# Optimization experiments

Hardware: AMD Instinct MI355X
Metric: run time of the kernel (lower is better)

The kernel has to match this reference:

```python
import jax, jax.numpy as jnp
import numpy as np

ROPE_BASE = 10000.0


def _rope(x):
    # x: (B, S, H, D) -- rotate-half RoPE applied per head over the sequence dim
    B, S, H, D = x.shape
    half = D // 2
    inv_freq = 1.0 / (ROPE_BASE ** (jnp.arange(half, dtype=jnp.float32) / half))
    ang = jnp.arange(S, dtype=jnp.float32)[:, None] * inv_freq[None, :]  # (S, half)
    cos = jnp.cos(ang)[None, :, None, :].astype(x.dtype)
    sin = jnp.sin(ang)[None, :, None, :].astype(x.dtype)
    x1, x2 = x[..., :half], x[..., half:]
    return jnp.concatenate([x1 * cos - x2 * sin, x2 * cos + x1 * sin], axis=-1)


def setup_inputs() -> dict:
    key = jax.random.key(0)
    ks = jax.random.split(key, 7)
    B, S, D = 8, 1024, 512
    HD = 512  # num_heads * key_dim = 8 * 64
    scale = 0.02
    return {
        "query": jax.random.normal(ks[0], (B, S, D), dtype=jnp.float32),
        "value": jax.random.normal(ks[1], (B, S, D), dtype=jnp.float32),
        "key_in": jax.random.normal(ks[2], (B, S, D), dtype=jnp.float32),
        "Wq": jax.random.normal(ks[3], (D, HD), dtype=jnp.float32) * scale,
        "Wk": jax.random.normal(ks[4], (D, HD), dtype=jnp.float32) * scale,
        "Wv": jax.random.normal(ks[5], (D, HD), dtype=jnp.float32) * scale,
        "Wo": jax.random.normal(ks[6], (HD, D), dtype=jnp.float32) * scale,
    }


def reference(query, value, key_in, Wq, Wk, Wv, Wo):
    H, Dh = 8, 64
    B, Sq, _ = query.shape
    Sk = key_in.shape[1]
    # QKV projections, split heads: (B, S, H, Dh)
    q = (query @ Wq).reshape(B, Sq, H, Dh)
    v = (value @ Wv).reshape(B, Sk, H, Dh)
    k = (key_in @ Wk).reshape(B, Sk, H, Dh)
    # inline RoPE on q and k (applied before head transpose, as in the original)
    q = _rope(q)
    k = _rope(k)
    # scaled dot-product attention with causal mask
    q = q * (1.0 / jnp.sqrt(jnp.asarray(Dh, q.dtype)))
    scores = jnp.einsum("bqhd,bkhd->bhqk", q, k)  # (B, H, Sq, Sk)
    causal = jnp.tril(jnp.ones((Sq, Sk), dtype=bool))[None, None]
    scores = jnp.where(causal, scores, jnp.asarray(-1e9, scores.dtype))
    probs = jax.nn.softmax(scores, axis=-1)
    out = jnp.einsum("bhqk,bkhd->bqhd", probs, v)  # (B, Sq, H, Dh)
    out = out.reshape(B, Sq, H * Dh) @ Wo  # output projection
    return out
```

## Files before the change

kernel.cpp:

```cpp
#include <hip/hip_runtime.h>
#include <hip/hip_bf16.h>
#include <stdint.h>

#define DEV static __device__ __forceinline__

typedef __attribute__((ext_vector_type(8)))  short    s16x8;
typedef __attribute__((ext_vector_type(4)))  short    s16x4;
typedef __attribute__((ext_vector_type(8)))  __bf16   bf16x8;
typedef __attribute__((ext_vector_type(4)))  float    f32x4;
typedef __attribute__((ext_vector_type(16))) float    f32x16;
typedef __attribute__((ext_vector_type(2)))  unsigned u32x2;
typedef __attribute__((ext_vector_type(4)))  unsigned u32x4;

DEV short f2b(float f){
  union{float f; uint32_t i;} x; x.f = f;
  uint32_t r = x.i + 0x7FFFu + ((x.i >> 16) & 1u);
  return (short)(r >> 16);
}
DEV bf16x8 as_bf(s16x8 v){ return __builtin_bit_cast(bf16x8, v); }
DEV float fexp2(float x){ return __builtin_amdgcn_exp2f(x); }
DEV f32x4 mf(s16x8 a, s16x8 b, f32x4 c){
  return __builtin_amdgcn_mfma_f32_16x16x32_bf16(as_bf(a), as_bf(b), c, 0, 0, 0);
}
DEV f32x16 mf32(s16x8 a, s16x8 b, f32x16 c){
  return __builtin_amdgcn_mfma_f32_32x32x16_bf16(as_bf(a), as_bf(b), c, 0, 0, 0);
}

DEV void gload_lds16(const void* g, void* l){
  __builtin_amdgcn_global_load_lds((const __attribute__((address_space(1))) void*)g,
                                   (__attribute__((address_space(3))) void*)l, 16, 0, 0);
}

#if __has_builtin(__builtin_amdgcn_permlane32_swap)
DEV void pswap2(unsigned a, unsigned b, unsigned& x, unsigned& y){
  u32x2 rr = __builtin_amdgcn_permlane32_swap(a, b, false, false);
  x = rr[0]; y = rr[1];
}
DEV float partner32(float v, int hi){
  unsigned u = __builtin_bit_cast(unsigned, v);
  u32x2 rr = __builtin_amdgcn_permlane32_swap(u, u, false, false);
  return __builtin_bit_cast(float, hi ? rr[0] : rr[1]);
}
#else
DEV void pswap2(unsigned a, unsigned b, unsigned& x, unsigned& y){
  unsigned pa_ = (unsigned)__shfl_xor((int)a, 32, 64);
  unsigned pb_ = (unsigned)__shfl_xor((int)b, 32, 64);
  int lo = ((threadIdx.x & 63) < 32);
  x = lo ? a   : pb_;
  y = lo ? pa_ : b;
}
DEV float partner32(float v, int hi){ (void)hi; return __shfl_xor(v, 32, 64); }
#endif

__global__ __launch_bounds__(256) void k_conv3(const float* __restrict__ q,
                                               const float* __restrict__ k,
                                               const float* __restrict__ v,
                                               short* __restrict__ out){
  int z = blockIdx.z;
  const float* in = (z == 0) ? q : (z == 1) ? k : v;
  int i = (blockIdx.x * 256 + threadIdx.x) * 4;
  float4 val = *(const float4*)(in + i);
  short o[4] = { f2b(val.x), f2b(val.y), f2b(val.z), f2b(val.w) };
  *(uint2*)(out + (size_t)z * 4194304 + i) = *(uint2*)o;
}

__global__ __launch_bounds__(256) void k_wt4(const float* __restrict__ w0,
                                             const float* __restrict__ w1,
                                             const float* __restrict__ w2,
                                             const float* __restrict__ w3,
                                             short* __restrict__ wt){
  __shared__ float tile[32][33];
  int z = blockIdx.z;
  const float* w = (z == 0) ? w0 : (z == 1) ? w1 : (z == 2) ? w2 : w3;
  short* o = wt + (size_t)z * 262144;
  int bx = blockIdx.x * 32, by = blockIdx.y * 32;
  int tx = threadIdx.x, ty = threadIdx.y;
  for (int j = 0; j < 32; j += 8)
    tile[ty + j][tx] = w[(size_t)(by + ty + j) * 512 + bx + tx];
  __syncthreads();
  for (int j = 0; j < 32; j += 8)
    o[(size_t)(bx + ty + j) * 512 + by + tx] = f2b(tile[tx][ty + j]);
}

__global__ __launch_bounds__(256) void k_table(float* __restrict__ tab){
  int idx = blockIdx.x * 256 + threadIdx.x;
  int s = idx >> 5, j = idx & 31;
  float inv = __expf(-(float)j * (1.0f / 32.0f) * logf(10000.0f));
  float ang = (float)s * inv;
  tab[idx * 2 + 0] = cosf(ang);
  tab[idx * 2 + 1] = sinf(ang);
}

__global__ __launch_bounds__(256) void k_qkv(const short* __restrict__ Xb,
                                             const short* __restrict__ Wcat,
                                             const float* __restrict__ tab,
                                             short* __restrict__ Qa,
                                             short* __restrict__ Ka,
                                             short* __restrict__ Vt){
  __shared__ __align__(16) short Al[2][4096];
  __shared__ __align__(16) short Bl[2][4096];
  const int t = threadIdx.x, w = t >> 6, lane = t & 63, fr = lane & 15, fg = lane >> 4;
  const int sel = blockIdx.y >> 2;
  const short* X = Xb + (size_t)sel * 4194304;
  const int bm = blockIdx.x * 128, bn = blockIdx.y * 128;
  const int wm = (w >> 1) * 64, wn = (w & 1) * 64;

  auto stage = [&](int buf, int k0){
#pragma unroll
    for (int q = 0; q < 2; q++){
      int lin = q * 256 + t;
      int row = lin >> 2, sl = lin & 3;
      int gs = (sl ^ (row & 3)) * 8;
      gload_lds16(X    + (size_t)(bm + row) * 512 + k0 + gs, &Al[buf][(q * 256 + w * 64) * 8]);
      gload_lds16(Wcat + (size_t)(bn + row) * 512 + k0 + gs, &Bl[buf][(q * 256 + w * 64) * 8]);
    }
  };

  f32x4 acc[4][4] = {};
  stage(0, 0);
  __syncthreads();
  int cur = 0;
  for (int t16 = 0; t16 < 16; ++t16){
    if (t16 < 15) stage(cur ^ 1, (t16 + 1) * 32);
    s16x8 af[4], bv[4];
#pragma unroll
    for (int f = 0; f < 4; f++){
      int ra = wm + f * 16 + fr;
      af[f] = *(const s16x8*)(&Al[cur][ra * 32 + ((fg ^ (ra & 3)) * 8)]);
      int rb = wn + f * 16 + fr;
      bv[f] = *(const s16x8*)(&Bl[cur][rb * 32 + ((fg ^ (rb & 3)) * 8)]);
    }
#pragma unroll
    for (int i = 0; i < 4; i++)
#pragma unroll
      for (int jj = 0; jj < 4; jj++)
        acc[i][jj] = mf(af[i], bv[jj], acc[i][jj]);
    __syncthreads();
    cur ^= 1;
  }

  const int row0 = bm + wm + fg * 4;
  const int b = row0 >> 10;
  const int s_base = row0 & 1023;
  const int hh = (((blockIdx.y & 3) * 128) + wn) >> 6;
  if (sel < 2){
    const float scale = (sel == 0) ? 0.125f * 1.44269504f : 1.0f;
    short* out = (sel == 0) ? Qa : Ka;
#pragma unroll
    for (int i = 0; i < 4; i++)
#pragma unroll
      for (int jj = 0; jj < 2; jj++){
        int d = jj * 16 + fr;
#pragma unroll
        for (int r = 0; r < 4; r++){
          int s = s_base + i * 16 + r;
          float2 cs = *(const float2*)(tab + (size_t)(s * 32 + d) * 2);
          float x1 = acc[i][jj][r], x2 = acc[i][jj + 2][r];
          size_t ob = ((size_t)((b * 8 + hh) * 1024 + s)) * 64 + d;
          out[ob]      = f2b((x1 * cs.x - x2 * cs.y) * scale);
          out[ob + 32] = f2b((x2 * cs.x + x1 * cs.y) * scale);
        }
      }
  } else {
#pragma unroll
    for (int i = 0; i < 4; i++)
#pragma unroll
      for (int jj = 0; jj < 4; jj++){
        int d = jj * 16 + fr;
        s16x4 pk;
#pragma unroll
        for (int r = 0; r < 4; r++) pk[r] = f2b(acc[i][jj][r]);
        size_t ob = ((size_t)((b * 8 + hh) * 64 + d)) * 1024 + s_base + i * 16;
        *(s16x4*)(Vt + ob) = pk;
      }
  }
}

__global__ __launch_bounds__(128) void k_attn(const short* __restrict__ Qb,
                                              const short* __restrict__ Kb,
                                              const short* __restrict__ Vt,
                                              short* __restrict__ O){
  __shared__ __align__(16) short KL[2][4096];
  __shared__ __align__(16) short VL[2][4096];
  const int bid = blockIdx.x;
  const int podr[16] = {15,14,13,12, 0,1,2,3, 11,10,9,8, 4,5,6,7};
  const int Bi = podr[bid >> 6];
  const int bh = bid & 63;
  const int B0 = Bi * 64;
  const int t = threadIdx.x, w = t >> 6, lane = t & 63;
  const int col = lane & 31, hi = lane >> 5;
  const short* Qp = Qb + (size_t)bh * 65536;
  const short* Kp = Kb + (size_t)bh * 65536;
  const short* Vp = Vt + (size_t)bh * 65536;
  const int qrow = B0 + 2 * col + w;

  s16x8 qb[4];
#pragma unroll
  for (int ks = 0; ks < 4; ks++)
    qb[ks] = *(const s16x8*)(Qp + (size_t)qrow * 64 + ks * 16 + hi * 8);

  int crow[16];
#pragma unroll
  for (int r = 0; r < 16; r++) crow[r] = (r & 3) + 8 * (r >> 2) + 4 * hi;

  f32x16 oacc[2] = {};
  float m = -1e30f, l = 0.f;

  auto stage = [&](int buf, int kv0){
#pragma unroll
    for (int R = 0; R < 4; R++){
      int lin = R * 128 + w * 64 + lane;
      int row = lin >> 3, slot = lin & 7;
      int gs = ((slot ^ (row & 7)) * 8);
      gload_lds16(Kp + (size_t)(kv0 + row) * 64 + gs, &KL[buf][(R * 128 + w * 64) * 8]);
      gload_lds16(Vp + (size_t)row * 1024 + kv0 + gs, &VL[buf][(R * 128 + w * 64) * 8]);
    }
  };

  stage(0, 0);
  __syncthreads();

  int cur = 0;
  for (int kv0 = 0; kv0 <= B0; kv0 += 64){
    if (kv0 < B0) stage(cur ^ 1, kv0 + 64);
    f32x16 sc[2];
#pragma unroll
    for (int f = 0; f < 2; f++){
      f32x16 s = {};
      int row = f * 32 + col, rx = row & 7;
#pragma unroll
      for (int ks = 0; ks < 4; ks++){
        s16x8 ka = *(const s16x8*)(&KL[cur][row * 64 + ((ks * 2 + hi) ^ rx) * 8]);
        s = mf32(ka, qb[ks], s);
      }
      sc[f] = s;
    }
    if (kv0 == B0){
#pragma unroll
      for (int f = 0; f < 2; f++)
#pragma unroll
        for (int r = 0; r < 16; r++){
          int kv = kv0 + f * 32 + crow[r];
          if (kv > qrow) sc[f][r] = -1e30f;
        }
    }
    float tm = -1e30f;
#pragma unroll
    for (int f = 0; f < 2; f++)
#pragma unroll
      for (int r = 0; r < 16; r++) tm = fmaxf(tm, sc[f][r]);
    tm = fmaxf(tm, partner32(tm, hi));
    if (!__all(tm <= m + 8.f)){
      float mn = fmaxf(m, tm);
      float corr = fexp2(m - mn);
      m = mn;
      l *= corr;
      float cpv[16];
#pragma unroll
      for (int r = 0; r < 16; r++) cpv[r] = __shfl(corr, crow[r], 64);
#pragma unroll
      for (int r = 0; r < 16; r++){ oacc[0][r] *= cpv[r]; oacc[1][r] *= cpv[r]; }
    }
    float rs = 0.f;
    unsigned wq[2][8];
#pragma unroll
    for (int f = 0; f < 2; f++)
#pragma unroll
      for (int i = 0; i < 8; i++){
        float p0 = fexp2(sc[f][2 * i]     - m);
        float p1 = fexp2(sc[f][2 * i + 1] - m);
        rs += p0 + p1;
        wq[f][i] = (unsigned)(uint16_t)f2b(p0) | ((unsigned)(uint16_t)f2b(p1) << 16);
      }
    rs += partner32(rs, hi);
    l += rs;
    s16x8 pa[4];
#pragma unroll
    for (int f = 0; f < 2; f++)
#pragma unroll
      for (int half = 0; half < 2; half++){
        unsigned w0, w1, w2, w3;
        pswap2(wq[f][half * 4 + 0], wq[f][half * 4 + 2], w0, w2);
        pswap2(wq[f][half * 4 + 1], wq[f][half * 4 + 3], w1, w3);
        u32x4 uv = { w0, w1, w2, w3 };
        pa[f * 2 + half] = __builtin_bit_cast(s16x8, uv);
      }
#pragma unroll
    for (int ks = 0; ks < 4; ks++)
#pragma unroll
      for (int df = 0; df < 2; df++){
        int row = df * 32 + col;
        s16x8 vb = *(const s16x8*)(&VL[cur][row * 64 + ((ks * 2 + hi) ^ (row & 7)) * 8]);
        oacc[df] = mf32(pa[ks], vb, oacc[df]);
      }
    if (kv0 < B0) __syncthreads();
    cur ^= 1;
  }

  const int b = bh >> 3, h = bh & 7;
  float lf[16];
#pragma unroll
  for (int r = 0; r < 16; r++) lf[r] = __shfl(l, crow[r], 64);
#pragma unroll
  for (int r = 0; r < 16; r++){
    int qq = B0 + 2 * crow[r] + w;
    float inv = 1.0f / lf[r];
    O[(size_t)(b * 1024 + qq) * 512 + h * 64 + col]      = f2b(oacc[0][r] * inv);
    O[(size_t)(b * 1024 + qq) * 512 + h * 64 + 32 + col] = f2b(oacc[1][r] * inv);
  }
}

__global__ __launch_bounds__(256, 2) void k_gemm_out(const short* __restrict__ X,
                                                     const short* __restrict__ Wt,
                                                     float* __restrict__ C){
  __shared__ __align__(16) short Al[2][8192];
  __shared__ __align__(16) short Bl[2][8192];
  const int t = threadIdx.x;
  const int w = t >> 6, lane = t & 63, fr = lane & 15, fg = lane >> 4;
  const int bm = blockIdx.x * 128, bn = blockIdx.y * 128;
  const int wm = (w >> 1) * 64, wn = (w & 1) * 64;

  auto stage = [&](int buf, int k0){
#pragma unroll
    for (int q = 0; q < 4; q++){
      int lin = q * 256 + t;
      int row = lin >> 3, sl = lin & 7;
      int gs = (sl ^ (row & 7)) * 8;
      gload_lds16(X  + (size_t)(bm + row) * 512 + k0 + gs, &Al[buf][(q * 256 + w * 64) * 8]);
      gload_lds16(Wt + (size_t)(bn + row) * 512 + k0 + gs, &Bl[buf][(q * 256 + w * 64) * 8]);
    }
  };

  f32x4 acc[4][4] = {};
  stage(0, 0);
  __syncthreads();
  int cur = 0;
  for (int t8 = 0; t8 < 8; ++t8){
    if (t8 < 7) stage(cur ^ 1, (t8 + 1) * 64);
#pragma unroll
    for (int kk = 0; kk < 2; kk++){
      s16x8 af[4], bv[4];
#pragma unroll
      for (int f = 0; f < 4; f++){
        int rowa = wm + f * 16 + fr;
        af[f] = *(const s16x8*)(&Al[cur][rowa * 64 + ((kk * 4 + fg) ^ (rowa & 7)) * 8]);
        int rowb = wn + f * 16 + fr;
        bv[f] = *(const s16x8*)(&Bl[cur][rowb * 64 + ((kk * 4 + fg) ^ (rowb & 7)) * 8]);
      }
#pragma unroll
      for (int i = 0; i < 4; i++)
#pragma unroll
        for (int jj = 0; jj < 4; jj++)
          acc[i][jj] = mf(af[i], bv[jj], acc[i][jj]);
    }
    __syncthreads();
    cur ^= 1;
  }
  const int row0 = bm + wm + fg * 4;
  const int col0 = bn + wn + fr;
#pragma unroll
  for (int i = 0; i < 4; i++)
#pragma unroll
    for (int jj = 0; jj < 4; jj++)
#pragma unroll
      for (int r = 0; r < 4; r++)
        C[(size_t)(row0 + i * 16 + r) * 512 + col0 + jj * 16] = acc[i][jj][r];
}

extern "C" void kernel_launch(void* const* d_in, const int* in_sizes, int n_in,
                              void* d_out, int out_size, void* d_ws, size_t ws_size,
                              hipStream_t stream){
  const float* query  = (const float*)d_in[0];
  const float* value  = (const float*)d_in[1];
  const float* key_in = (const float*)d_in[2];
  const float* Wq     = (const float*)d_in[3];
  const float* Wk     = (const float*)d_in[4];
  const float* Wv     = (const float*)d_in[5];
  const float* Wo     = (const float*)d_in[6];

  char* ws = (char*)d_ws;
  const size_t MB = 1ull << 20;
  short* Xb   = (short*)(ws);
  short* Wcat = (short*)(ws + 24 * MB);
  float* tab  = (float*)(ws + 26 * MB);
  short* Qa   = (short*)(ws + 26 * MB + 256 * 1024);
  short* Ka   = (short*)((char*)Qa + 8 * MB);
  short* Va   = (short*)((char*)Ka + 8 * MB);
  short* Oa   = Xb;
  short* Wot  = Wcat + 786432;

  k_conv3<<<dim3(4096, 1, 3), 256, 0, stream>>>(query, key_in, value, Xb);
  k_wt4<<<dim3(16, 16, 4), dim3(32, 8), 0, stream>>>(Wq, Wk, Wv, Wo, Wcat);
  k_table<<<128, 256, 0, stream>>>(tab);

  k_qkv<<<dim3(64, 12), 256, 0, stream>>>(Xb, Wcat, tab, Qa, Ka, Va);

  k_attn<<<1024, 128, 0, stream>>>(Qa, Ka, Va, Oa);

  k_gemm_out<<<dim3(64, 4), 256, 0, stream>>>(Oa, Wot, (float*)d_out);
}
```

Baseline: 85.19 us.

## Double attention query tile to 128 rows with four waves per block

The attention kernel now runs 256-thread blocks that each handle 128 query rows instead of 64, so every staged K/V tile is reused by four waves and the grid drops to 512 blocks. The block-order map and the causal masking for the last two tiles are adjusted to match. Max and sum reductions become tree reductions, the bf16 packing uses a native conversion, and s_setprio raises wave priority around the MFMA sections. The larger tile halves K/V traffic per query row, but it also halves the block count and adds a second masked tile at the diagonal.

```diff
diff --git a/kernel.cpp b/kernel.cpp
--- a/kernel.cpp
+++ b/kernel.cpp
@@ -7,6 +7,7 @@
 typedef __attribute__((ext_vector_type(8)))  short    s16x8;
 typedef __attribute__((ext_vector_type(4)))  short    s16x4;
 typedef __attribute__((ext_vector_type(8)))  __bf16   bf16x8;
+typedef __attribute__((ext_vector_type(2)))  __bf16   bf16x2;
 typedef __attribute__((ext_vector_type(4)))  float    f32x4;
 typedef __attribute__((ext_vector_type(16))) float    f32x16;
 typedef __attribute__((ext_vector_type(2)))  unsigned u32x2;
@@ -16,6 +17,10 @@
   union{float f; uint32_t i;} x; x.f = f;
   uint32_t r = x.i + 0x7FFFu + ((x.i >> 16) & 1u);
   return (short)(r >> 16);
+}
+DEV unsigned packbf(float a, float b){
+  bf16x2 v = { (__bf16)a, (__bf16)b };
+  return __builtin_bit_cast(unsigned, v);
 }
 DEV bf16x8 as_bf(s16x8 v){ return __builtin_bit_cast(bf16x8, v); }
 DEV float fexp2(float x){ return __builtin_amdgcn_exp2f(x); }
@@ -176,23 +181,24 @@
   }
 }
 
-__global__ __launch_bounds__(128) void k_attn(const short* __restrict__ Qb,
+__global__ __launch_bounds__(256) void k_attn(const short* __restrict__ Qb,
                                               const short* __restrict__ Kb,
                                               const short* __restrict__ Vt,
                                               short* __restrict__ O){
   __shared__ __align__(16) short KL[2][4096];
   __shared__ __align__(16) short VL[2][4096];
   const int bid = blockIdx.x;
-  const int podr[16] = {15,14,13,12, 0,1,2,3, 11,10,9,8, 4,5,6,7};
-  const int Bi = podr[bid >> 6];
+  const int BiMap[8] = {7,6,5,4, 0,1,2,3};
+  const int Bi = BiMap[bid >> 6];
   const int bh = bid & 63;
-  const int B0 = Bi * 64;
+  const int B0 = Bi * 128;
+  const int KVEND = B0 + 128;
   const int t = threadIdx.x, w = t >> 6, lane = t & 63;
   const int col = lane & 31, hi = lane >> 5;
   const short* Qp = Qb + (size_t)bh * 65536;
   const short* Kp = Kb + (size_t)bh * 65536;
   const short* Vp = Vt + (size_t)bh * 65536;
-  const int qrow = B0 + 2 * col + w;
+  const int qrow = B0 + 4 * col + w;
 
   s16x8 qb[4];
 #pragma unroll
@@ -208,12 +214,12 @@
 
   auto stage = [&](int buf, int kv0){
 #pragma unroll
-    for (int R = 0; R < 4; R++){
-      int lin = R * 128 + w * 64 + lane;
+    for (int R = 0; R < 2; R++){
+      int lin = R * 256 + w * 64 + lane;
       int row = lin >> 3, slot = lin & 7;
       int gs = ((slot ^ (row & 7)) * 8);
-      gload_lds16(Kp + (size_t)(kv0 + row) * 64 + gs, &KL[buf][(R * 128 + w * 64) * 8]);
-      gload_lds16(Vp + (size_t)row * 1024 + kv0 + gs, &VL[buf][(R * 128 + w * 64) * 8]);
+      gload_lds16(Kp + (size_t)(kv0 + row) * 64 + gs, &KL[buf][(R * 256 + w * 64) * 8]);
+      gload_lds16(Vp + (size_t)row * 1024 + kv0 + gs, &VL[buf][(R * 256 + w * 64) * 8]);
     }
   };
 
@@ -221,8 +227,10 @@
   __syncthreads();
 
   int cur = 0;
-  for (int kv0 = 0; kv0 <= B0; kv0 += 64){
-    if (kv0 < B0) stage(cur ^ 1, kv0 + 64);
+  for (int kv0 = 0; kv0 < KVEND; kv0 += 64){
+    const bool hasNext = (kv0 + 64 < KVEND);
+    if (hasNext) stage(cur ^ 1, kv0 + 64);
+    __builtin_amdgcn_s_setprio(1);
     f32x16 sc[2];
 #pragma unroll
     for (int f = 0; f < 2; f++){
@@ -235,7 +243,8 @@
       }
       sc[f] = s;
     }
-    if (kv0 == B0){
+    __builtin_amdgcn_s_setprio(0);
+    if (kv0 >= B0){
 #pragma unroll
       for (int f = 0; f < 2; f++)
 #pragma unroll
@@ -244,12 +253,14 @@
           if (kv > qrow) sc[f][r] = -1e30f;
         }
     }
-    float tm = -1e30f;
-#pragma unroll
-    for (int f = 0; f < 2; f++)
-#pragma unroll
-      for (int r = 0; r < 16; r++) tm = fmaxf(tm, sc[f][r]);
-    tm = fmaxf(tm, partner32(tm, hi));
+    float mx[16];
+#pragma unroll
+    for (int r = 0; r < 16; r++) mx[r] = fmaxf(sc[0][r], sc[1][r]);
+#pragma unroll
+    for (int off = 8; off >= 1; off >>= 1)
+#pragma unroll
+      for (int r = 0; r < off; r++) mx[r] = fmaxf(mx[r], mx[r + off]);
+    float tm = fmaxf(mx[0], partner32(mx[0], hi));
     if (!__all(tm <= m + 8.f)){
       float mn = fmaxf(m, tm);
       float corr = fexp2(m - mn);
@@ -261,19 +272,22 @@
 #pragma unroll
       for (int r = 0; r < 16; r++){ oacc[0][r] *= cpv[r]; oacc[1][r] *= cpv[r]; }
     }
-    float rs = 0.f;
+    float p[32];
+#pragma unroll
+    for (int f = 0; f < 2; f++)
+#pragma unroll
+      for (int i = 0; i < 16; i++) p[f * 16 + i] = fexp2(sc[f][i] - m);
     unsigned wq[2][8];
 #pragma unroll
     for (int f = 0; f < 2; f++)
 #pragma unroll
-      for (int i = 0; i < 8; i++){
-        float p0 = fexp2(sc[f][2 * i]     - m);
-        float p1 = fexp2(sc[f][2 * i + 1] - m);
-        rs += p0 + p1;
-        wq[f][i] = (unsigned)(uint16_t)f2b(p0) | ((unsigned)(uint16_t)f2b(p1) << 16);
-      }
-    rs += partner32(rs, hi);
-    l += rs;
+      for (int i = 0; i < 8; i++)
+        wq[f][i] = packbf(p[f * 16 + 2 * i], p[f * 16 + 2 * i + 1]);
+#pragma unroll
+    for (int off = 16; off >= 1; off >>= 1)
+#pragma unroll
+      for (int r = 0; r < off; r++) p[r] += p[r + off];
+    l += p[0] + partner32(p[0], hi);
     s16x8 pa[4];
 #pragma unroll
     for (int f = 0; f < 2; f++)
@@ -285,6 +299,7 @@
         u32x4 uv = { w0, w1, w2, w3 };
         pa[f * 2 + half] = __builtin_bit_cast(s16x8, uv);
       }
+    __builtin_amdgcn_s_setprio(1);
 #pragma unroll
     for (int ks = 0; ks < 4; ks++)
 #pragma unroll
@@ -293,7 +308,8 @@
         s16x8 vb = *(const s16x8*)(&VL[cur][row * 64 + ((ks * 2 + hi) ^ (row & 7)) * 8]);
         oacc[df] = mf32(pa[ks], vb, oacc[df]);
       }
-    if (kv0 < B0) __syncthreads();
+    __builtin_amdgcn_s_setprio(0);
+    if (hasNext) __syncthreads();
     cur ^= 1;
   }
 
@@ -303,7 +319,7 @@
   for (int r = 0; r < 16; r++) lf[r] = __shfl(l, crow[r], 64);
 #pragma unroll
   for (int r = 0; r < 16; r++){
-    int qq = B0 + 2 * crow[r] + w;
+    int qq = B0 + 4 * crow[r] + w;
     float inv = 1.0f / lf[r];
     O[(size_t)(b * 1024 + qq) * 512 + h * 64 + col]      = f2b(oacc[0][r] * inv);
     O[(size_t)(b * 1024 + qq) * 512 + h * 64 + 32 + col] = f2b(oacc[1][r] * inv);
@@ -395,7 +411,7 @@
 
   k_qkv<<<dim3(64, 12), 256, 0, stream>>>(Xb, Wcat, tab, Qa, Ka, Va);
 
-  k_attn<<<1024, 128, 0, stream>>>(Qa, Ka, Va, Oa);
+  k_attn<<<512, 256, 0, stream>>>(Qa, Ka, Va, Oa);
 
   k_gemm_out<<<dim3(64, 4), 256, 0, stream>>>(Oa, Wot, (float*)d_out);
 }
```

Result: no change. 83.97 us (-1.4%).

## Fuse fp32-to-bf16 input conversion into QKV GEMM; triple-buffer GEMM pipelines

Applied to the files above, without the earlier changes.

Removes the separate conversion kernel, so the QKV projection now loads the fp32 activations through registers, converts them to bf16 and writes them into LDS itself. This saves a full write and re-read of the bf16 copy of the inputs, plus one kernel launch. Both the QKV and output GEMMs move to a three-stage LDS pipeline with explicit vmcnt waits and raw barriers, so more loads stay in flight. The cost is more LDS use and register pressure, and dropping launch_bounds(256,2) on the output GEMM may lower occupancy. Each QKV block now re-reads fp32 A tiles, which is twice the bytes of the bf16 copy.

```diff
diff --git a/kernel.cpp b/kernel.cpp
--- a/kernel.cpp
+++ b/kernel.cpp
@@ -12,6 +12,14 @@
 typedef __attribute__((ext_vector_type(2)))  unsigned u32x2;
 typedef __attribute__((ext_vector_type(4)))  unsigned u32x4;
 
+#define WAIT_VMCNT(N) do{ asm volatile("s_waitcnt vmcnt(" #N ")" ::: "memory"); \
+                          __builtin_amdgcn_sched_barrier(0); }while(0)
+DEV void barrier_full(){
+  asm volatile("s_waitcnt lgkmcnt(0)" ::: "memory");
+  __builtin_amdgcn_sched_barrier(0);
+  __builtin_amdgcn_s_barrier();
+}
+
 DEV short f2b(float f){
   union{float f; uint32_t i;} x; x.f = f;
   uint32_t r = x.i + 0x7FFFu + ((x.i >> 16) & 1u);
@@ -51,18 +59,6 @@
 }
 DEV float partner32(float v, int hi){ (void)hi; return __shfl_xor(v, 32, 64); }
 #endif
-
-__global__ __launch_bounds__(256) void k_conv3(const float* __restrict__ q,
-                                               const float* __restrict__ k,
-                                               const float* __restrict__ v,
-                                               short* __restrict__ out){
-  int z = blockIdx.z;
-  const float* in = (z == 0) ? q : (z == 1) ? k : v;
-  int i = (blockIdx.x * 256 + threadIdx.x) * 4;
-  float4 val = *(const float4*)(in + i);
-  short o[4] = { f2b(val.x), f2b(val.y), f2b(val.z), f2b(val.w) };
-  *(uint2*)(out + (size_t)z * 4194304 + i) = *(uint2*)o;
-}
 
 __global__ __launch_bounds__(256) void k_wt4(const float* __restrict__ w0,
                                              const float* __restrict__ w1,
@@ -91,52 +87,81 @@
   tab[idx * 2 + 1] = sinf(ang);
 }
 
-__global__ __launch_bounds__(256) void k_qkv(const short* __restrict__ Xb,
+__global__ __launch_bounds__(256) void k_qkv(const float* __restrict__ Xq,
+                                             const float* __restrict__ Xk,
+                                             const float* __restrict__ Xv,
                                              const short* __restrict__ Wcat,
                                              const float* __restrict__ tab,
                                              short* __restrict__ Qa,
                                              short* __restrict__ Ka,
                                              short* __restrict__ Vt){
-  __shared__ __align__(16) short Al[2][4096];
-  __shared__ __align__(16) short Bl[2][4096];
+  __shared__ __align__(16) short Al[3][4096];
+  __shared__ __align__(16) short Bl[3][4096];
   const int t = threadIdx.x, w = t >> 6, lane = t & 63, fr = lane & 15, fg = lane >> 4;
   const int sel = blockIdx.y >> 2;
-  const short* X = Xb + (size_t)sel * 4194304;
+  const float* X = (sel == 0) ? Xq : (sel == 1) ? Xk : Xv;
   const int bm = blockIdx.x * 128, bn = blockIdx.y * 128;
   const int wm = (w >> 1) * 64, wn = (w & 1) * 64;
 
-  auto stage = [&](int buf, int k0){
+  auto stageB = [&](int buf, int k0){
 #pragma unroll
     for (int q = 0; q < 2; q++){
       int lin = q * 256 + t;
       int row = lin >> 2, sl = lin & 3;
       int gs = (sl ^ (row & 3)) * 8;
-      gload_lds16(X    + (size_t)(bm + row) * 512 + k0 + gs, &Al[buf][(q * 256 + w * 64) * 8]);
       gload_lds16(Wcat + (size_t)(bn + row) * 512 + k0 + gs, &Bl[buf][(q * 256 + w * 64) * 8]);
     }
   };
+  auto ldA = [&](float4 (&dst)[4], int k0){
+    const float* s0 = X + (size_t)(bm + (t >> 2)) * 512 + k0 + (t & 3) * 8;
+    const float* s1 = s0 + 64 * 512;
+    dst[0] = *(const float4*)(s0);
+    dst[1] = *(const float4*)(s0 + 4);
+    dst[2] = *(const float4*)(s1);
+    dst[3] = *(const float4*)(s1 + 4);
+  };
+  auto wrA = [&](int buf, float4 (&src)[4]){
+    s16x8 p0 = { f2b(src[0].x), f2b(src[0].y), f2b(src[0].z), f2b(src[0].w),
+                 f2b(src[1].x), f2b(src[1].y), f2b(src[1].z), f2b(src[1].w) };
+    s16x8 p1 = { f2b(src[2].x), f2b(src[2].y), f2b(src[2].z), f2b(src[2].w),
+                 f2b(src[3].x), f2b(src[3].y), f2b(src[3].z), f2b(src[3].w) };
+    int r0 = t >> 2, sl = t & 3, sw = (sl ^ (r0 & 3)) * 8;
+    *(s16x8*)(&Al[buf][r0 * 32 + sw])        = p0;
+    *(s16x8*)(&Al[buf][(64 + r0) * 32 + sw]) = p1;
+  };
 
   f32x4 acc[4][4] = {};
-  stage(0, 0);
-  __syncthreads();
-  int cur = 0;
-  for (int t16 = 0; t16 < 16; ++t16){
-    if (t16 < 15) stage(cur ^ 1, (t16 + 1) * 32);
+  float4 uaA[4], uaB[4];
+  stageB(0, 0); stageB(1, 32);
+  ldA(uaB, 0); ldA(uaA, 32);
+  WAIT_VMCNT(4);
+  wrA(0, uaB);
+
+  auto body = [&](int i, float4 (&cur)[4], float4 (&nxt)[4]){
+    barrier_full();
+    int kc = i + 2; if (kc > 15) kc = 15;
+    stageB((i + 2) % 3, kc * 32);
+    ldA(nxt, kc * 32);
+    WAIT_VMCNT(6);
+    wrA((i + 1) % 3, cur);
+    const int curb = i % 3;
     s16x8 af[4], bv[4];
 #pragma unroll
     for (int f = 0; f < 4; f++){
       int ra = wm + f * 16 + fr;
-      af[f] = *(const s16x8*)(&Al[cur][ra * 32 + ((fg ^ (ra & 3)) * 8)]);
+      af[f] = *(const s16x8*)(&Al[curb][ra * 32 + ((fg ^ (ra & 3)) * 8)]);
       int rb = wn + f * 16 + fr;
-      bv[f] = *(const s16x8*)(&Bl[cur][rb * 32 + ((fg ^ (rb & 3)) * 8)]);
-    }
-#pragma unroll
-    for (int i = 0; i < 4; i++)
+      bv[f] = *(const s16x8*)(&Bl[curb][rb * 32 + ((fg ^ (rb & 3)) * 8)]);
+    }
+#pragma unroll
+    for (int i2 = 0; i2 < 4; i2++)
 #pragma unroll
       for (int jj = 0; jj < 4; jj++)
-        acc[i][jj] = mf(af[i], bv[jj], acc[i][jj]);
-    __syncthreads();
-    cur ^= 1;
+        acc[i2][jj] = mf(af[i2], bv[jj], acc[i2][jj]);
+  };
+  for (int i = 0; i < 16; i += 2){
+    body(i,     uaA, uaB);
+    body(i + 1, uaB, uaA);
   }
 
   const int row0 = bm + wm + fg * 4;
@@ -310,11 +335,11 @@
   }
 }
 
-__global__ __launch_bounds__(256, 2) void k_gemm_out(const short* __restrict__ X,
-                                                     const short* __restrict__ Wt,
-                                                     float* __restrict__ C){
-  __shared__ __align__(16) short Al[2][8192];
-  __shared__ __align__(16) short Bl[2][8192];
+__global__ __launch_bounds__(256) void k_gemm_out(const short* __restrict__ X,
+                                                  const short* __restrict__ Wt,
+                                                  float* __restrict__ C){
+  __shared__ __align__(16) short Al[3][8192];
+  __shared__ __align__(16) short Bl[3][8192];
   const int t = threadIdx.x;
   const int w = t >> 6, lane = t & 63, fr = lane & 15, fg = lane >> 4;
   const int bm = blockIdx.x * 128, bn = blockIdx.y * 128;
@@ -333,10 +358,13 @@
 
   f32x4 acc[4][4] = {};
   stage(0, 0);
-  __syncthreads();
-  int cur = 0;
+  stage(1, 64);
   for (int t8 = 0; t8 < 8; ++t8){
-    if (t8 < 7) stage(cur ^ 1, (t8 + 1) * 64);
+    WAIT_VMCNT(8);
+    __builtin_amdgcn_s_barrier();
+    int kc = t8 + 2; if (kc > 7) kc = 7;
+    stage((t8 + 2) % 3, kc * 64);
+    const int cur = t8 % 3;
 #pragma unroll
     for (int kk = 0; kk < 2; kk++){
       s16x8 af[4], bv[4];
@@ -353,8 +381,6 @@
         for (int jj = 0; jj < 4; jj++)
           acc[i][jj] = mf(af[i], bv[jj], acc[i][jj]);
     }
-    __syncthreads();
-    cur ^= 1;
   }
   const int row0 = bm + wm + fg * 4;
   const int col0 = bn + wn + fr;
@@ -380,20 +406,18 @@
 
   char* ws = (char*)d_ws;
   const size_t MB = 1ull << 20;
-  short* Xb   = (short*)(ws);
+  short* Oa   = (short*)(ws);
   short* Wcat = (short*)(ws + 24 * MB);
   float* tab  = (float*)(ws + 26 * MB);
   short* Qa   = (short*)(ws + 26 * MB + 256 * 1024);
   short* Ka   = (short*)((char*)Qa + 8 * MB);
   short* Va   = (short*)((char*)Ka + 8 * MB);
-  short* Oa   = Xb;
   short* Wot  = Wcat + 786432;
 
-  k_conv3<<<dim3(4096, 1, 3), 256, 0, stream>>>(query, key_in, value, Xb);
   k_wt4<<<dim3(16, 16, 4), dim3(32, 8), 0, stream>>>(Wq, Wk, Wv, Wo, Wcat);
   k_table<<<128, 256, 0, stream>>>(tab);
 
-  k_qkv<<<dim3(64, 12), 256, 0, stream>>>(Xb, Wcat, tab, Qa, Ka, Va);
+  k_qkv<<<dim3(64, 12), 256, 0, stream>>>(query, key_in, value, Wcat, tab, Qa, Ka, Va);
 
   k_attn<<<1024, 128, 0, stream>>>(Qa, Ka, Va, Oa);
 
```

Result: no change. 86.49 us (+1.5%).
